# Performance work log

Hardware: AMD Instinct MI355X
Metric: run time of the kernel (lower is better)

Reference implementation:

```python
import jax, jax.numpy as jnp
import numpy as np

N_NODES = 100000
N_EDGES = 1600000
IN_FEATS = 128
HIDDEN = 128


def _graph_conv(x, W, b, src, dst, n_nodes):
    # DGL GraphConv with norm='both': out = D_in^{-1/2} * A^T * (D_out^{-1/2} * x) @ W + b
    ones = jnp.ones((src.shape[0],), dtype=x.dtype)
    deg_out = jax.ops.segment_sum(ones, src, num_segments=n_nodes)
    deg_in = jax.ops.segment_sum(ones, dst, num_segments=n_nodes)
    norm_src = jax.lax.rsqrt(jnp.clip(deg_out, 1.0))  # [N]
    norm_dst = jax.lax.rsqrt(jnp.clip(deg_in, 1.0))   # [N]
    h = x @ W                                          # [N, F_out]
    msg = h[src] * norm_src[src][:, None]              # gather by edge src: [E, F_out]
    agg = jax.ops.segment_sum(msg, dst, num_segments=n_nodes)  # scatter-add to dst
    return agg * norm_dst[:, None] + b


def setup_inputs() -> dict:
    key = jax.random.key(0)
    ks = jax.random.split(key, 9)
    x = jax.random.normal(ks[0], (N_NODES, IN_FEATS), dtype=jnp.float32)
    src = jax.random.randint(ks[1], (N_EDGES,), 0, N_NODES, dtype=jnp.int32)
    dst = jax.random.randint(ks[2], (N_EDGES,), 0, N_NODES, dtype=jnp.int32)
    s1 = 1.0 / np.sqrt(IN_FEATS)
    s2 = 1.0 / np.sqrt(HIDDEN)
    W1 = jax.random.uniform(ks[3], (IN_FEATS, HIDDEN), jnp.float32, -s1, s1)
    b1 = jnp.zeros((HIDDEN,), jnp.float32)
    W2 = jax.random.uniform(ks[4], (HIDDEN, HIDDEN), jnp.float32, -s2, s2)
    b2 = jnp.zeros((HIDDEN,), jnp.float32)
    sp = 1.0 / np.sqrt(2 * HIDDEN)
    Wp = jax.random.uniform(ks[5], (2 * HIDDEN, 1), jnp.float32, -sp, sp)
    bp = jax.random.uniform(ks[6], (1,), jnp.float32, -sp, sp)
    return {"x": x, "W1": W1, "b1": b1, "W2": W2, "b2": b2,
            "Wp": Wp, "bp": bp, "src": src, "dst": dst}


def reference(x, W1, b1, W2, b2, Wp, bp, src, dst):
    n_nodes = x.shape[0]
    h = _graph_conv(x, W1, b1, src, dst, n_nodes)
    h = jax.nn.relu(h)
    h = _graph_conv(h, W2, b2, src, dst, n_nodes)  # final node embeddings [N, H]
    # predict_links on the same edge list: cat(h[u], h[v]) -> linear -> sigmoid
    edge_h = jnp.concatenate([h[src], h[dst]], axis=1)  # [E, 2H]
    scores = jax.nn.sigmoid(edge_h @ Wp + bp)           # [E, 1]
    return scores
```

## Files before the change

kernel.cpp:

```cpp
#include <hip/hip_runtime.h>
#include <cstdint>
#include <cstddef>

#define NN 100000
#define NE 1600000
#define F  128
#define NPAD 100352
#define NBUCK 3125
#define BCAPG 768
#define NFILL 1536
#define NGEMM 1024
#define CHUNK 1042
#define GSTRIDE 16
#define NREG 49
#define RCAP 36864
#define P2SPLIT 16
#define P2MAX 2304

typedef __attribute__((ext_vector_type(8))) short bf16x8;
typedef __attribute__((ext_vector_type(4))) float f32x4;

__device__ __forceinline__ unsigned short f2bf(float f) {
    unsigned u = __float_as_uint(f);
    unsigned r = (u + 0x7fffu + ((u >> 16) & 1u)) >> 16;
    return (unsigned short)r;
}
__device__ __forceinline__ void acc_bf8s(const uint4 v, const float ns, float* acc) {
    acc[0] += __uint_as_float(v.x << 16) * ns;
    acc[1] += __uint_as_float(v.x & 0xffff0000u) * ns;
    acc[2] += __uint_as_float(v.y << 16) * ns;
    acc[3] += __uint_as_float(v.y & 0xffff0000u) * ns;
    acc[4] += __uint_as_float(v.z << 16) * ns;
    acc[5] += __uint_as_float(v.z & 0xffff0000u) * ns;
    acc[6] += __uint_as_float(v.w << 16) * ns;
    acc[7] += __uint_as_float(v.w & 0xffff0000u) * ns;
}

__global__ void setup_kernel(int* __restrict__ gCur, int* __restrict__ gRegCur,
                             const float* __restrict__ W2, const float* __restrict__ Wp,
                             const float* __restrict__ b2, const float* __restrict__ bp,
                             float* __restrict__ consts, float2* __restrict__ V) {
    const int g = blockIdx.x;
    const int tid = threadIdx.x;
    if (g < 13) {
        const int b = g * 256 + tid;
        if (b < NBUCK) gCur[b * GSTRIDE] = b * BCAPG;
        return;
    }
    if (tid < 128) {
        float sa = 0.f, sc = 0.f;
        #pragma unroll 8
        for (int j = 0; j < F; ++j) {
            const float w = W2[tid * F + j];
            sa += w * Wp[j];
            sc += w * Wp[F + j];
        }
        V[tid] = make_float2(sa, sc);
    } else if (tid < 192) {
        const int l = tid - 128;
        const float2 bb = *(const float2*)&b2[2 * l];
        const float2 wa = *(const float2*)&Wp[2 * l];
        const float2 wc = *(const float2*)&Wp[F + 2 * l];
        float s = bb.x * (wa.x + wc.x) + bb.y * (wa.y + wc.y);
        #pragma unroll
        for (int m = 32; m > 0; m >>= 1) s += __shfl_xor(s, m);
        if (l == 0) consts[0] = s + bp[0];
    } else if (tid < 192 + NREG) {
        const int r = tid - 192;
        gRegCur[r * GSTRIDE] = r * RCAP;
    }
}

__global__ __launch_bounds__(256, 8)
void fill_kernel(const int* __restrict__ src, const int* __restrict__ dst,
                 int* __restrict__ deg_out, int* __restrict__ gRegCur,
                 int* __restrict__ gRegion) {
    __shared__ int sortedL[CHUNK];
    __shared__ unsigned char regOf[CHUNK];
    __shared__ int cnt[NREG], cur[NREG], base[NREG];

    const int g = blockIdx.x;
    const int tid = threadIdx.x;

    const int e0 = g * CHUNK;
    const int nCh = min(CHUNK, NE - e0);
    if (tid < NREG) cnt[tid] = 0;
    __syncthreads();
    for (int i = tid; i < nCh; i += 256) {
        const int s = src[e0 + i];
        const int d = dst[e0 + i];
        atomicAdd(&deg_out[s], 1);
        atomicAdd(&cnt[d >> 11], 1);
    }
    __syncthreads();
    if (tid < NREG && cnt[tid] > 0)
        base[tid] = atomicAdd(&gRegCur[tid * GSTRIDE], cnt[tid]);
    if (tid == 0) {
        int run = 0;
        for (int r = 0; r < NREG; ++r) { cur[r] = run; run += cnt[r]; }
    }
    __syncthreads();
    for (int i = tid; i < nCh; i += 256) {
        const int s = src[e0 + i];
        const int d = dst[e0 + i];
        const int r = d >> 11;
        const int p = atomicAdd(&cur[r], 1);
        sortedL[p] = s | ((d & 0x7FF) << 17);
        regOf[p] = (unsigned char)r;
    }
    __syncthreads();
    for (int i = tid; i < nCh; i += 256) {
        const int r = regOf[i];
        const int start = cur[r] - cnt[r];
        const int dstAbs = base[r] + (i - start);
        if (dstAbs < (r + 1) * RCAP)
            gRegion[dstAbs] = sortedL[i];
    }
}

__global__ __launch_bounds__(256, 4)
void gemm1_kernel(const float* __restrict__ in, const float* __restrict__ W,
                  unsigned short* __restrict__ out_bf) {
    __shared__ __align__(16) char A_s[8192];

    const int g    = blockIdx.x;
    const int tid  = threadIdx.x;
    const int w    = tid >> 6;
    const int lane = tid & 63;
    const int ml   = lane & 15;
    const int quad = lane >> 4;

    bf16x8 Bf[4][2];
    #pragma unroll
    for (int kb = 0; kb < 4; ++kb) {
        #pragma unroll
        for (int nb = 0; nb < 2; ++nb) {
            const int n = 32 * w + nb * 16 + ml;
            const int k0 = kb * 32 + quad * 8;
            #pragma unroll
            for (int j = 0; j < 8; ++j)
                Bf[kb][nb][j] = (short)f2bf(W[(k0 + j) * F + n]);
        }
    }

    const int nTiles = NN / 32;
    for (int tile = g; tile < nTiles; tile += NGEMM) {
        const int row0 = tile * 32;
        __syncthreads();
        #pragma unroll
        for (int c = 0; c < 2; ++c) {
            const int i2 = tid + 256 * c;
            const int m  = i2 >> 4;
            const int o  = i2 & 15;
            const float* xr = &in[(size_t)(row0 + m) * F + o * 8];
            const float4 v0 = *(const float4*)xr;
            const float4 v1 = *(const float4*)(xr + 4);
            short h8[8];
            h8[0] = (short)f2bf(v0.x); h8[1] = (short)f2bf(v0.y);
            h8[2] = (short)f2bf(v0.z); h8[3] = (short)f2bf(v0.w);
            h8[4] = (short)f2bf(v1.x); h8[5] = (short)f2bf(v1.y);
            h8[6] = (short)f2bf(v1.z); h8[7] = (short)f2bf(v1.w);
            const int kb2 = o >> 2, q2 = o & 3, ml2 = m & 15, mh2 = m >> 4;
            const int fo = (((mh2 * 4 + kb2) * 64) + q2 * 16 + ml2) * 16;
            *(bf16x8*)(A_s + fo) = *(bf16x8*)h8;
        }
        __syncthreads();

        f32x4 acc00 = {0,0,0,0}, acc01 = {0,0,0,0}, acc10 = {0,0,0,0}, acc11 = {0,0,0,0};
        #pragma unroll
        for (int kb = 0; kb < 4; ++kb) {
            const bf16x8 ah0 = *(const bf16x8*)(A_s + (kb * 64 + lane) * 16);
            const bf16x8 ah1 = *(const bf16x8*)(A_s + ((4 + kb) * 64 + lane) * 16);
            acc00 = __builtin_amdgcn_mfma_f32_16x16x32_bf16(ah0, Bf[kb][0], acc00, 0, 0, 0);
            acc01 = __builtin_amdgcn_mfma_f32_16x16x32_bf16(ah0, Bf[kb][1], acc01, 0, 0, 0);
            acc10 = __builtin_amdgcn_mfma_f32_16x16x32_bf16(ah1, Bf[kb][0], acc10, 0, 0, 0);
            acc11 = __builtin_amdgcn_mfma_f32_16x16x32_bf16(ah1, Bf[kb][1], acc11, 0, 0, 0);
        }

        #pragma unroll
        for (int mh = 0; mh < 2; ++mh) {
            #pragma unroll
            for (int nb = 0; nb < 2; ++nb) {
                const f32x4 a = (mh == 0) ? (nb == 0 ? acc00 : acc01)
                                          : (nb == 0 ? acc10 : acc11);
                const int row = row0 + mh * 16 + quad * 4;
                const int col = 32 * w + nb * 16 + ml;
                #pragma unroll
                for (int r = 0; r < 4; ++r)
                    out_bf[(size_t)(row + r) * F + col] = f2bf(a[r]);
            }
        }
    }
}

__global__ __launch_bounds__(256)
void pass2_kernel(const int* __restrict__ gRegion, const int* __restrict__ gRegCur,
                  int* __restrict__ gCur, int* __restrict__ srcPart,
                  const int* __restrict__ deg_out, float* __restrict__ norm_src) {
    __shared__ int sortedL[P2MAX];
    __shared__ unsigned char fbOf[P2MAX];
    __shared__ int cnt[64], cur[64], base[64];

    const int r   = blockIdx.x / P2SPLIT;
    const int j   = blockIdx.x % P2SPLIT;
    const int tid = threadIdx.x;

    {
        const int n = blockIdx.x * 128 + tid;
        if (tid < 128 && n < NN)
            norm_src[n] = rsqrtf((float)max(deg_out[n], 1));
    }

    const int total = min(gRegCur[r * GSTRIDE] - r * RCAP, RCAP);
    const int per = (total + P2SPLIT - 1) / P2SPLIT;
    const int i0 = j * per;
    const int i1 = min(total, i0 + per);
    const int n = i1 - i0;

    if (tid < 64) cnt[tid] = 0;
    __syncthreads();

    int v[9];
    #pragma unroll
    for (int k = 0; k < 9; ++k) {
        const int i = tid + k * 256;
        if (i < n) {
            const int vv = gRegion[r * RCAP + i0 + i];
            v[k] = vv;
            atomicAdd(&cnt[vv >> 22], 1);
        }
    }
    __syncthreads();
    if (tid < 64 && cnt[tid] > 0)
        base[tid] = atomicAdd(&gCur[(r * 64 + tid) * GSTRIDE], cnt[tid]);
    if (tid == 0) {
        int run = 0;
        for (int f = 0; f < 64; ++f) { cur[f] = run; run += cnt[f]; }
    }
    __syncthreads();
    #pragma unroll
    for (int k = 0; k < 9; ++k) {
        const int i = tid + k * 256;
        if (i < n) {
            const int fb = v[k] >> 22;
            const int p = atomicAdd(&cur[fb], 1);
            sortedL[p] = v[k] & 0x3FFFFF;
            fbOf[p] = (unsigned char)fb;
        }
    }
    __syncthreads();
    for (int i = tid; i < n; i += 256) {
        const int fb = fbOf[i];
        const int start = cur[fb] - cnt[fb];
        const int dstAbs = base[fb] + (i - start);
        if (dstAbs < (r * 64 + fb + 1) * BCAPG)
            srcPart[dstAbs] = sortedL[i];
    }
}

__global__ __launch_bounds__(256)
void gather_sort_kernel(const unsigned short* __restrict__ hs,
                        int* __restrict__ srcPart, const int* __restrict__ gCur,
                        const float* __restrict__ norm_src, const float* __restrict__ bias,
                        const float2* __restrict__ V, float2* __restrict__ uw,
                        int* __restrict__ offs, int* __restrict__ ends,
                        float* __restrict__ norm_dst) {
    __shared__ int cnt[32];
    __shared__ int loc[32];
    __shared__ int cur[32];
    __shared__ int sortedL[BCAPG];

    const int b   = blockIdx.x;
    const int tid = threadIdx.x;
    const int nlo = b * 32;
    const int nCnt = min(32, NN - nlo);
    const int eBase = b * BCAPG;
    const int total = min(gCur[b * GSTRIDE] - eBase, BCAPG);

    if (tid < 32) cnt[tid] = 0;
    __syncthreads();
    for (int i = tid; i < total; i += 256)
        atomicAdd(&cnt[(srcPart[eBase + i] >> 17) & 31], 1);
    __syncthreads();
    if (tid < 32) loc[tid] = cnt[tid];
    __syncthreads();
    for (int off = 1; off < 32; off <<= 1) {
        int v = 0;
        if (tid < 32 && tid >= off) v = loc[tid - off];
        __syncthreads();
        if (tid < 32) loc[tid] += v;
        __syncthreads();
    }
    if (tid < 32) cur[tid] = loc[tid] - cnt[tid];
    if (tid < nCnt) {
        const int st = eBase + loc[tid] - cnt[tid];
        offs[nlo + tid] = st;
        ends[nlo + tid] = st + cnt[tid];
        norm_dst[nlo + tid] = rsqrtf((float)max(cnt[tid], 1));
    }
    __syncthreads();
    for (int i = tid; i < total; i += 256) {
        const int v = srcPart[eBase + i];
        const int r = atomicAdd(&cur[(v >> 17) & 31], 1);
        sortedL[r] = v & 0x1FFFF;
    }
    __syncthreads();
    for (int i = tid; i < total; i += 256)
        srcPart[eBase + i] = sortedL[i];

    const int w  = tid >> 6;
    const int l  = tid & 63;
    const int q  = l >> 4;
    const int c8 = (l & 15) * 8;
    float bb[8];
    *(float4*)&bb[0] = *(const float4*)&bias[c8];
    *(float4*)&bb[4] = *(const float4*)&bias[c8 + 4];
    float2 Vl[8];
    #pragma unroll
    for (int k = 0; k < 8; ++k) Vl[k] = V[c8 + k];

    const int nhEnd = min((w + 1) * 8, nCnt);
    for (int nh = w * 8; nh < nhEnd; ++nh) {
        const int end = loc[nh];
        const int beg = end - cnt[nh];
        float acc[8] = {0.f, 0.f, 0.f, 0.f, 0.f, 0.f, 0.f, 0.f};
        int j = beg;
        for (; j + 16 <= end; j += 16) {
            const int s0 = sortedL[j + q];
            const int s1 = sortedL[j + 4 + q];
            const int s2 = sortedL[j + 8 + q];
            const int s3 = sortedL[j + 12 + q];
            const float ns0 = norm_src[s0];
            const float ns1 = norm_src[s1];
            const float ns2 = norm_src[s2];
            const float ns3 = norm_src[s3];
            const uint4 v0 = *(const uint4*)&hs[(size_t)s0 * F + c8];
            const uint4 v1 = *(const uint4*)&hs[(size_t)s1 * F + c8];
            const uint4 v2 = *(const uint4*)&hs[(size_t)s2 * F + c8];
            const uint4 v3 = *(const uint4*)&hs[(size_t)s3 * F + c8];
            acc_bf8s(v0, ns0, acc);
            acc_bf8s(v1, ns1, acc);
            acc_bf8s(v2, ns2, acc);
            acc_bf8s(v3, ns3, acc);
        }
        for (; j + 8 <= end; j += 8) {
            const int s0 = sortedL[j + q];
            const int s1 = sortedL[j + 4 + q];
            const float ns0 = norm_src[s0];
            const float ns1 = norm_src[s1];
            const uint4 v0 = *(const uint4*)&hs[(size_t)s0 * F + c8];
            const uint4 v1 = *(const uint4*)&hs[(size_t)s1 * F + c8];
            acc_bf8s(v0, ns0, acc);
            acc_bf8s(v1, ns1, acc);
        }
        for (; j + 4 <= end; j += 4) {
            const int s = sortedL[j + q];
            const float ns = norm_src[s];
            const uint4 v = *(const uint4*)&hs[(size_t)s * F + c8];
            acc_bf8s(v, ns, acc);
        }
        if (j + q < end) {
            const int s = sortedL[j + q];
            const float ns = norm_src[s];
            const uint4 v = *(const uint4*)&hs[(size_t)s * F + c8];
            acc_bf8s(v, ns, acc);
        }
        #pragma unroll
        for (int k = 0; k < 8; ++k) {
            acc[k] += __shfl_xor(acc[k], 16);
            acc[k] += __shfl_xor(acc[k], 32);
        }

        const int n = nlo + nh;
        const float nd = rsqrtf((float)max(cnt[nh], 1));
        float pa = 0.f, pc = 0.f;
        #pragma unroll
        for (int k = 0; k < 8; ++k) {
            const float ok = fmaxf(acc[k] * nd + bb[k], 0.f);
            pa += ok * Vl[k].x;
            pc += ok * Vl[k].y;
        }
        #pragma unroll
        for (int m = 1; m <= 8; m <<= 1) {
            pa += __shfl_xor(pa, m);
            pc += __shfl_xor(pc, m);
        }
        if (l == 0) {
            const float ns = norm_src[n];
            uw[n] = make_float2(ns * pa, ns * pc);
        }
    }
}

__global__ void ac_kernel(const float2* __restrict__ uw, const int* __restrict__ sorted_src,
                          const int* __restrict__ offs, const int* __restrict__ ends,
                          const float* __restrict__ norm_dst,
                          float* __restrict__ A, float* __restrict__ C, int nN) {
    const int n = blockIdx.x * blockDim.x + threadIdx.x;
    if (n >= nN) return;
    const int beg = offs[n];
    const int end = ends[n];
    float su = 0.f, sw = 0.f;
    int j = beg;
    for (; j + 2 <= end; j += 2) {
        const float2 t0 = uw[sorted_src[j]];
        const float2 t1 = uw[sorted_src[j + 1]];
        su += t0.x + t1.x;
        sw += t0.y + t1.y;
    }
    if (j < end) {
        const float2 t = uw[sorted_src[j]];
        su += t.x;
        sw += t.y;
    }
    const float nd = norm_dst[n];
    A[n] = nd * su;
    C[n] = nd * sw;
}

__global__ void score_kernel(const float* __restrict__ A, const float* __restrict__ C,
                             const int4* __restrict__ src4, const int4* __restrict__ dst4,
                             const float* __restrict__ consts, float4* __restrict__ out4,
                             int nE4) {
    const int i = blockIdx.x * blockDim.x + threadIdx.x;
    if (i < nE4) {
        const int4 s = src4[i];
        const int4 d = dst4[i];
        const float cc = consts[0];
        float4 o;
        o.x = 1.f / (1.f + __expf(-(A[s.x] + C[d.x] + cc)));
        o.y = 1.f / (1.f + __expf(-(A[s.y] + C[d.y] + cc)));
        o.z = 1.f / (1.f + __expf(-(A[s.z] + C[d.z] + cc)));
        o.w = 1.f / (1.f + __expf(-(A[s.w] + C[d.w] + cc)));
        out4[i] = o;
    }
}

extern "C" void kernel_launch(void* const* d_in, const int* in_sizes, int n_in,
                              void* d_out, int out_size, void* d_ws, size_t ws_size,
                              hipStream_t stream) {
    const float* x  = (const float*)d_in[0];
    const float* W1 = (const float*)d_in[1];
    const float* b1 = (const float*)d_in[2];
    const float* W2 = (const float*)d_in[3];
    const float* b2 = (const float*)d_in[4];
    const float* Wp = (const float*)d_in[5];
    const float* bp = (const float*)d_in[6];
    const int*   src = (const int*)d_in[7];
    const int*   dst = (const int*)d_in[8];
    float* out = (float*)d_out;

    float* ws        = (float*)d_ws;
    float* norm_src  = ws;
    float* bufA      = ws + NPAD;
    float* bufC      = ws + 2 * NPAD;
    float* norm_dst  = ws + 3 * NPAD;
    int*   offs      = (int*)(ws + 4 * NPAD);
    int*   ends      = offs + NPAD;
    int*   gCur      = ends + NPAD;
    int*   gRegCur   = gCur + 50176;
    float* consts    = (float*)(gRegCur + 1024);
    float2* V        = (float2*)(consts + 16);
    float2* uw       = V + 128;
    int*   srcPart   = (int*)(uw + NN);
    unsigned short* hs_bf = (unsigned short*)(srcPart + (size_t)NBUCK * BCAPG);
    int*   gRegion   = (int*)(hs_bf + (size_t)NN * F);

    hipMemsetAsync(bufA, 0, NPAD * sizeof(int), stream);
    setup_kernel<<<14, 256, 0, stream>>>(gCur, gRegCur, W2, Wp, b2, bp, consts, V);

    fill_kernel<<<NFILL, 256, 0, stream>>>(src, dst, (int*)bufA, gRegCur, gRegion);

    gemm1_kernel<<<NGEMM, 256, 0, stream>>>(x, W1, hs_bf);

    pass2_kernel<<<NREG * P2SPLIT, 256, 0, stream>>>(gRegion, gRegCur, gCur, srcPart,
                                                     (const int*)bufA, norm_src);

    gather_sort_kernel<<<NBUCK, 256, 0, stream>>>(hs_bf, srcPart, gCur, norm_src, b1,
                                                  V, uw, offs, ends, norm_dst);

    ac_kernel<<<(NN + 255) / 256, 256, 0, stream>>>(uw, srcPart, offs, ends, norm_dst,
                                                    bufA, bufC, NN);

    score_kernel<<<(NE / 4 + 255) / 256, 256, 0, stream>>>(bufA, bufC, (const int4*)src,
                                                           (const int4*)dst, consts,
                                                           (float4*)out, NE / 4);
}
```

Before: 339.5 us.

## Compute out-degree via region-bucketed src lists and shared-memory histograms

```diff
diff --git a/kernel.cpp b/kernel.cpp
--- a/kernel.cpp
+++ b/kernel.cpp
@@ -15,6 +15,7 @@
 #define NREG 49
 #define RCAP 36864
 #define P2SPLIT 16
+#define P2J 17
 #define P2MAX 2304
 
 typedef __attribute__((ext_vector_type(8))) short bf16x8;
@@ -37,6 +38,7 @@
 }
 
 __global__ void setup_kernel(int* __restrict__ gCur, int* __restrict__ gRegCur,
+                             int* __restrict__ gRegCurS,
                              const float* __restrict__ W2, const float* __restrict__ Wp,
                              const float* __restrict__ b2, const float* __restrict__ bp,
                              float* __restrict__ consts, float2* __restrict__ V) {
@@ -47,6 +49,14 @@
         if (b < NBUCK) gCur[b * GSTRIDE] = b * BCAPG;
         return;
     }
+    if (g == 14) {
+        if (tid < NREG) gRegCur[tid * GSTRIDE] = tid * RCAP;
+        else if (tid >= 64 && tid < 64 + NREG) {
+            const int r = tid - 64;
+            gRegCurS[r * GSTRIDE] = r * RCAP;
+        }
+        return;
+    }
     if (tid < 128) {
         float sa = 0.f, sc = 0.f;
         #pragma unroll 8
@@ -65,33 +75,26 @@
         #pragma unroll
         for (int m = 32; m > 0; m >>= 1) s += __shfl_xor(s, m);
         if (l == 0) consts[0] = s + bp[0];
-    } else if (tid < 192 + NREG) {
-        const int r = tid - 192;
-        gRegCur[r * GSTRIDE] = r * RCAP;
     }
 }
 
 __global__ __launch_bounds__(256, 8)
 void fill_kernel(const int* __restrict__ src, const int* __restrict__ dst,
-                 int* __restrict__ deg_out, int* __restrict__ gRegCur,
-                 int* __restrict__ gRegion) {
+                 int* __restrict__ gRegCur, int* __restrict__ gRegCurS,
+                 int* __restrict__ gRegion, unsigned short* __restrict__ gRegionS) {
     __shared__ int sortedL[CHUNK];
     __shared__ unsigned char regOf[CHUNK];
     __shared__ int cnt[NREG], cur[NREG], base[NREG];
 
     const int g = blockIdx.x;
     const int tid = threadIdx.x;
-
     const int e0 = g * CHUNK;
     const int nCh = min(CHUNK, NE - e0);
+
     if (tid < NREG) cnt[tid] = 0;
     __syncthreads();
-    for (int i = tid; i < nCh; i += 256) {
-        const int s = src[e0 + i];
-        const int d = dst[e0 + i];
-        atomicAdd(&deg_out[s], 1);
-        atomicAdd(&cnt[d >> 11], 1);
-    }
+    for (int i = tid; i < nCh; i += 256)
+        atomicAdd(&cnt[dst[e0 + i] >> 11], 1);
     __syncthreads();
     if (tid < NREG && cnt[tid] > 0)
         base[tid] = atomicAdd(&gRegCur[tid * GSTRIDE], cnt[tid]);
@@ -111,10 +114,37 @@
     __syncthreads();
     for (int i = tid; i < nCh; i += 256) {
         const int r = regOf[i];
-        const int start = cur[r] - cnt[r];
-        const int dstAbs = base[r] + (i - start);
+        const int dstAbs = base[r] + (i - (cur[r] - cnt[r]));
         if (dstAbs < (r + 1) * RCAP)
             gRegion[dstAbs] = sortedL[i];
+    }
+    __syncthreads();
+
+    if (tid < NREG) cnt[tid] = 0;
+    __syncthreads();
+    for (int i = tid; i < nCh; i += 256)
+        atomicAdd(&cnt[src[e0 + i] >> 11], 1);
+    __syncthreads();
+    if (tid < NREG && cnt[tid] > 0)
+        base[tid] = atomicAdd(&gRegCurS[tid * GSTRIDE], cnt[tid]);
+    if (tid == 0) {
+        int run = 0;
+        for (int r = 0; r < NREG; ++r) { cur[r] = run; run += cnt[r]; }
+    }
+    __syncthreads();
+    for (int i = tid; i < nCh; i += 256) {
+        const int s = src[e0 + i];
+        const int r = s >> 11;
+        const int p = atomicAdd(&cur[r], 1);
+        sortedL[p] = s;
+        regOf[p] = (unsigned char)r;
+    }
+    __syncthreads();
+    for (int i = tid; i < nCh; i += 256) {
+        const int r = regOf[i];
+        const int dstAbs = base[r] + (i - (cur[r] - cnt[r]));
+        if (dstAbs < (r + 1) * RCAP)
+            gRegionS[dstAbs] = (unsigned short)(sortedL[i] & 0x7FF);
     }
 }
 
@@ -194,22 +224,37 @@
 }
 
 __global__ __launch_bounds__(256)
-void pass2_kernel(const int* __restrict__ gRegion, const int* __restrict__ gRegCur,
+void pass2_kernel(const int* __restrict__ gRegion, const unsigned short* __restrict__ gRegionS,
+                  const int* __restrict__ gRegCur, const int* __restrict__ gRegCurS,
                   int* __restrict__ gCur, int* __restrict__ srcPart,
-                  const int* __restrict__ deg_out, float* __restrict__ norm_src) {
-    __shared__ int sortedL[P2MAX];
-    __shared__ unsigned char fbOf[P2MAX];
-    __shared__ int cnt[64], cur[64], base[64];
-
-    const int r   = blockIdx.x / P2SPLIT;
-    const int j   = blockIdx.x % P2SPLIT;
+                  float* __restrict__ norm_src) {
+    __shared__ __align__(16) char smem[12544];
+
+    const int r   = blockIdx.x / P2J;
+    const int j   = blockIdx.x % P2J;
     const int tid = threadIdx.x;
 
-    {
-        const int n = blockIdx.x * 128 + tid;
-        if (tid < 128 && n < NN)
-            norm_src[n] = rsqrtf((float)max(deg_out[n], 1));
-    }
+    if (j == P2SPLIT) {
+        int* hist = (int*)smem;
+        const int total = min(gRegCurS[r * GSTRIDE] - r * RCAP, RCAP);
+        for (int t = tid; t < 2048; t += 256) hist[t] = 0;
+        __syncthreads();
+        for (int i = tid; i < total; i += 256)
+            atomicAdd(&hist[gRegionS[r * RCAP + i]], 1);
+        __syncthreads();
+        const int nlo = r * 2048;
+        for (int t = tid; t < 2048; t += 256) {
+            const int n = nlo + t;
+            if (n < NN) norm_src[n] = rsqrtf((float)max(hist[t], 1));
+        }
+        return;
+    }
+
+    int* sortedL = (int*)smem;
+    unsigned char* fbOf = (unsigned char*)(smem + 9216);
+    int* cnt  = (int*)(smem + 11520);
+    int* cur  = cnt + 64;
+    int* base = cur + 64;
 
     const int total = min(gRegCur[r * GSTRIDE] - r * RCAP, RCAP);
     const int per = (total + P2SPLIT - 1) / P2SPLIT;
@@ -251,8 +296,7 @@
     __syncthreads();
     for (int i = tid; i < n; i += 256) {
         const int fb = fbOf[i];
-        const int start = cur[fb] - cnt[fb];
-        const int dstAbs = base[fb] + (i - start);
+        const int dstAbs = base[fb] + (i - (cur[fb] - cnt[fb]));
         if (dstAbs < (r * 64 + fb + 1) * BCAPG)
             srcPart[dstAbs] = sortedL[i];
     }
@@ -459,22 +503,23 @@
     int*   ends      = offs + NPAD;
     int*   gCur      = ends + NPAD;
     int*   gRegCur   = gCur + 50176;
-    float* consts    = (float*)(gRegCur + 1024);
+    int*   gRegCurS  = gRegCur + 1024;
+    float* consts    = (float*)(gRegCurS + 1024);
     float2* V        = (float2*)(consts + 16);
     float2* uw       = V + 128;
     int*   srcPart   = (int*)(uw + NN);
     unsigned short* hs_bf = (unsigned short*)(srcPart + (size_t)NBUCK * BCAPG);
     int*   gRegion   = (int*)(hs_bf + (size_t)NN * F);
-
-    hipMemsetAsync(bufA, 0, NPAD * sizeof(int), stream);
-    setup_kernel<<<14, 256, 0, stream>>>(gCur, gRegCur, W2, Wp, b2, bp, consts, V);
-
-    fill_kernel<<<NFILL, 256, 0, stream>>>(src, dst, (int*)bufA, gRegCur, gRegion);
+    unsigned short* gRegionS = (unsigned short*)(gRegion + (size_t)NREG * RCAP);
+
+    setup_kernel<<<15, 256, 0, stream>>>(gCur, gRegCur, gRegCurS, W2, Wp, b2, bp, consts, V);
+
+    fill_kernel<<<NFILL, 256, 0, stream>>>(src, dst, gRegCur, gRegCurS, gRegion, gRegionS);
 
     gemm1_kernel<<<NGEMM, 256, 0, stream>>>(x, W1, hs_bf);
 
-    pass2_kernel<<<NREG * P2SPLIT, 256, 0, stream>>>(gRegion, gRegCur, gCur, srcPart,
-                                                     (const int*)bufA, norm_src);
+    pass2_kernel<<<NREG * P2J, 256, 0, stream>>>(gRegion, gRegionS, gRegCur, gRegCurS,
+                                                 gCur, srcPart, norm_src);
 
     gather_sort_kernel<<<NBUCK, 256, 0, stream>>>(hs_bf, srcPart, gCur, norm_src, b1,
                                                   V, uw, offs, ends, norm_dst);
```

New measurement: 330.4 us. -2.7%, faster.
